# Kernel optimization log

Hardware: AMD Instinct MI355X
Metric: run time of the kernel (lower is better)

## Reference

```python
import jax, jax.numpy as jnp
import numpy as np

# Token / dim constants (from vm_step.Token and vm_step._SetDim)
CODE_START, CODE_END, MEM = 256, 257, 258
ADDR_KEY, MEM_STORE = 206, 455
VOCAB, D_MODEL = 272, 512
B, S = 16, 8192


def setup_inputs() -> dict:
    key = jax.random.key(0)
    k1, k2 = jax.random.split(key)
    token_ids = jax.random.randint(k1, (B, S), 0, VOCAB)
    embed_weight = jax.random.normal(k2, (VOCAB, D_MODEL), dtype=jnp.float32) * 0.02
    return {"token_ids": token_ids, "embed_weight": embed_weight, "mem_history_end": 2048}


def _augment_mask(token_ids, mem_history_end):
    """Boolean [B, S, D_MODEL] mask of positions that get set to 1.0."""
    Bb, Ss = token_ids.shape
    idx = jnp.arange(Ss)                                  # [S]
    is_start = token_ids == CODE_START
    is_end = token_ids == CODE_END
    # loop breaks at the FIRST CODE_END in each row
    end_idx = jnp.min(jnp.where(is_end, idx[None, :], Ss), axis=1)      # [B]
    # cs_pos = index of most recent CODE_START at-or-before i (-1 if none)
    cs = jax.lax.cummax(jnp.where(is_start, idx[None, :], -1), axis=1)  # [B,S]
    addr = idx[None, :] - cs - 1                                        # [B,S]
    valid = (cs >= 0) & (idx[None, :] < end_idx[:, None]) \
            & (token_ids < 256) & (addr >= 0)
    lo = addr & 15
    hi = (addr >> 4) & 15
    top = (addr >> 8) & 15
    bins = jnp.arange(16)                                 # nibble one-hots
    lo_oh = (bins == lo[..., None]) & valid[..., None]    # [B,S,16]
    hi_oh = (bins == hi[..., None]) & valid[..., None]
    top_oh = (bins == top[..., None]) & valid[..., None]
    mem_flag = (token_ids == MEM) & (idx[None, :] < mem_history_end)    # [B,S]

    mask = jnp.zeros((Bb, Ss, D_MODEL), dtype=bool)
    mask = mask.at[:, :, ADDR_KEY:ADDR_KEY + 16].set(lo_oh)
    mask = mask.at[:, :, ADDR_KEY + 16:ADDR_KEY + 32].set(hi_oh)
    mask = mask.at[:, :, ADDR_KEY + 32:ADDR_KEY + 48].set(top_oh)
    mask = mask.at[:, :, MEM_STORE].set(mem_flag)
    return mask


def reference(token_ids, embed_weight, mem_history_end):
    x = embed_weight[token_ids]                           # [B,S,D] gather
    mask = _augment_mask(token_ids, mem_history_end)
    return jnp.where(mask, jnp.asarray(1.0, x.dtype), x)
```

## Files before the change

kernel.cpp:

```cpp
#include <hip/hip_runtime.h>

#define TOK_CODE_START 256
#define TOK_CODE_END   257
#define TOK_MEM        258
#define ADDR_KEY       206
#define MEM_STORE      455

constexpr int Bb = 16;
constexpr int Ss = 8192;
constexpr int DM = 512;

__global__ __launch_bounds__(1024) void vm_scan_kernel(
    const int* __restrict__ tok,
    const int* __restrict__ mhe_p,
    unsigned int* __restrict__ ws)
{
    const int b = blockIdx.x;
    const int t = threadIdx.x;
    const int mhe = mhe_p[0];
    const int* row = tok + b * Ss;
    const int base = t * 8;

    int toks[8];
    int4 v0 = reinterpret_cast<const int4*>(row + base)[0];
    int4 v1 = reinterpret_cast<const int4*>(row + base)[1];
    toks[0] = v0.x; toks[1] = v0.y; toks[2] = v0.z; toks[3] = v0.w;
    toks[4] = v1.x; toks[5] = v1.y; toks[6] = v1.z; toks[7] = v1.w;

    int lmax = -1;
    int lend = Ss;
    #pragma unroll
    for (int k = 0; k < 8; ++k) {
        int idx = base + k;
        if (toks[k] == TOK_CODE_START) lmax = idx;
        if (toks[k] == TOK_CODE_END && lend == Ss) lend = idx;
    }

    __shared__ int smax[1024];
    __shared__ int smin[1024];
    smax[t] = lmax;
    smin[t] = lend;
    __syncthreads();

    for (int off = 512; off > 0; off >>= 1) {
        if (t < off) smin[t] = min(smin[t], smin[t + off]);
        __syncthreads();
    }
    const int end_idx = smin[0];

    for (int off = 1; off < 1024; off <<= 1) {
        int u = (t >= off) ? smax[t - off] : -1;
        __syncthreads();
        if (u > smax[t]) smax[t] = u;
        __syncthreads();
    }
    int run = (t > 0) ? smax[t - 1] : -1;

    unsigned int pk[8];
    #pragma unroll
    for (int k = 0; k < 8; ++k) {
        int idx = base + k;
        int tv = toks[k];
        if (tv == TOK_CODE_START) run = idx;
        int cs = run;
        int addr = idx - cs - 1;
        bool valid = (cs >= 0) && (idx < end_idx) && (tv < 256) && (addr >= 0);
        bool memf  = (tv == TOK_MEM) && (idx < mhe);
        unsigned int w = (valid ? 1u : 0u) | (memf ? 2u : 0u);
        if (valid) w |= ((unsigned int)addr << 2);
        pk[k] = w;
    }
    uint4* wr = reinterpret_cast<uint4*>(ws + b * Ss + base);
    wr[0] = make_uint4(pk[0], pk[1], pk[2], pk[3]);
    wr[1] = make_uint4(pk[4], pk[5], pk[6], pk[7]);
}

__global__ __launch_bounds__(256) void vm_gather_kernel(
    const int* __restrict__ tok,
    const float* __restrict__ emb,
    const unsigned int* __restrict__ ws,
    float4* __restrict__ out)
{
    const long long total = (long long)Bb * Ss * (DM / 4);
    const long long stride = (long long)gridDim.x * blockDim.x;
    for (long long w = (long long)blockIdx.x * blockDim.x + threadIdx.x;
         w < total; w += stride) {
        int bs = (int)(w >> 7);
        int dq = (int)(w & 127);
        int d0 = dq << 2;
        int tk = tok[bs];
        unsigned int pw = ws[bs];
        float4 v = reinterpret_cast<const float4*>(emb)[tk * (DM / 4) + dq];
        if (pw) {
            bool valid = (pw & 1u) != 0u;
            bool memf  = (pw & 2u) != 0u;
            int addr = (int)(pw >> 2);
            int p0 = ADDR_KEY      + (addr & 15);
            int p1 = ADDR_KEY + 16 + ((addr >> 4) & 15);
            int p2 = ADDR_KEY + 32 + ((addr >> 8) & 15);
            int d;
            d = d0 + 0; if ((valid && (d == p0 || d == p1 || d == p2)) || (memf && d == MEM_STORE)) v.x = 1.0f;
            d = d0 + 1; if ((valid && (d == p0 || d == p1 || d == p2)) || (memf && d == MEM_STORE)) v.y = 1.0f;
            d = d0 + 2; if ((valid && (d == p0 || d == p1 || d == p2)) || (memf && d == MEM_STORE)) v.z = 1.0f;
            d = d0 + 3; if ((valid && (d == p0 || d == p1 || d == p2)) || (memf && d == MEM_STORE)) v.w = 1.0f;
        }
        out[w] = v;
    }
}

extern "C" void kernel_launch(void* const* d_in, const int* in_sizes, int n_in,
                              void* d_out, int out_size, void* d_ws, size_t ws_size,
                              hipStream_t stream) {
    const int* tok = (const int*)d_in[0];
    const float* emb = (const float*)d_in[1];
    const int* mhe = (const int*)d_in[2];
    unsigned int* ws = (unsigned int*)d_ws;
    float4* out = (float4*)d_out;

    vm_scan_kernel<<<Bb, 1024, 0, stream>>>(tok, mhe, ws);
    vm_gather_kernel<<<2048, 256, 0, stream>>>(tok, emb, ws, out);
}
```

Before: 53.27 us.

## Use wave-shuffle scan, pack token into workspace word, nontemporal output stores

The scan kernel replaces its shared-memory Hillis-Steele scan and tree reduction, which need many __syncthreads, with wave-level shuffle scans plus a small cross-wave combine. The workspace word now also carries the token id, so the gather kernel no longer reads the token array. The gather uses 32-bit indexing and nontemporal stores for the 268MB output to reduce cache pollution. The gather is dominated by output write bandwidth, so these changes may matter little. The packing assumes token ids fit in 9 bits.

```diff
diff --git a/kernel.cpp b/kernel.cpp
--- a/kernel.cpp
+++ b/kernel.cpp
@@ -10,6 +10,8 @@
 constexpr int Ss = 8192;
 constexpr int DM = 512;
 
+typedef float f32x4 __attribute__((ext_vector_type(4)));
+
 __global__ __launch_bounds__(1024) void vm_scan_kernel(
     const int* __restrict__ tok,
     const int* __restrict__ mhe_p,
@@ -17,6 +19,8 @@
 {
     const int b = blockIdx.x;
     const int t = threadIdx.x;
+    const int lane = t & 63;
+    const int wid = t >> 6;
     const int mhe = mhe_p[0];
     const int* row = tok + b * Ss;
     const int base = t * 8;
@@ -36,25 +40,36 @@
         if (toks[k] == TOK_CODE_END && lend == Ss) lend = idx;
     }
 
-    __shared__ int smax[1024];
-    __shared__ int smin[1024];
-    smax[t] = lmax;
-    smin[t] = lend;
+    #pragma unroll
+    for (int off = 1; off < 64; off <<= 1) {
+        int u = __shfl_up(lmax, off);
+        if (lane >= off && u > lmax) lmax = u;
+    }
+    int excl = __shfl_up(lmax, 1);
+    if (lane == 0) excl = -1;
+
+    #pragma unroll
+    for (int off = 32; off > 0; off >>= 1) {
+        int u = __shfl_xor(lend, off);
+        if (u < lend) lend = u;
+    }
+
+    __shared__ int wmax[16];
+    __shared__ int wend[16];
+    if (lane == 63) wmax[wid] = lmax;
+    if (lane == 0)  wend[wid] = lend;
     __syncthreads();
 
-    for (int off = 512; off > 0; off >>= 1) {
-        if (t < off) smin[t] = min(smin[t], smin[t + off]);
-        __syncthreads();
-    }
-    const int end_idx = smin[0];
+    int carry = -1;
+    #pragma unroll
+    for (int j = 0; j < 16; ++j)
+        if (j < wid && wmax[j] > carry) carry = wmax[j];
+    int end_idx = Ss;
+    #pragma unroll
+    for (int j = 0; j < 16; ++j)
+        if (wend[j] < end_idx) end_idx = wend[j];
 
-    for (int off = 1; off < 1024; off <<= 1) {
-        int u = (t >= off) ? smax[t - off] : -1;
-        __syncthreads();
-        if (u > smax[t]) smax[t] = u;
-        __syncthreads();
-    }
-    int run = (t > 0) ? smax[t - 1] : -1;
+    int run = (carry > excl) ? carry : excl;
 
     unsigned int pk[8];
     #pragma unroll
@@ -66,8 +81,9 @@
         int addr = idx - cs - 1;
         bool valid = (cs >= 0) && (idx < end_idx) && (tv < 256) && (addr >= 0);
         bool memf  = (tv == TOK_MEM) && (idx < mhe);
-        unsigned int w = (valid ? 1u : 0u) | (memf ? 2u : 0u);
-        if (valid) w |= ((unsigned int)addr << 2);
+        unsigned int w = (unsigned int)tv;
+        if (valid) w |= (1u << 9) | ((unsigned int)addr << 11);
+        if (memf)  w |= (1u << 10);
         pk[k] = w;
     }
     uint4* wr = reinterpret_cast<uint4*>(ws + b * Ss + base);
@@ -76,35 +92,35 @@
 }
 
 __global__ __launch_bounds__(256) void vm_gather_kernel(
-    const int* __restrict__ tok,
-    const float* __restrict__ emb,
+    const f32x4* __restrict__ emb,
     const unsigned int* __restrict__ ws,
-    float4* __restrict__ out)
+    f32x4* __restrict__ out)
 {
-    const long long total = (long long)Bb * Ss * (DM / 4);
-    const long long stride = (long long)gridDim.x * blockDim.x;
-    for (long long w = (long long)blockIdx.x * blockDim.x + threadIdx.x;
-         w < total; w += stride) {
-        int bs = (int)(w >> 7);
-        int dq = (int)(w & 127);
-        int d0 = dq << 2;
-        int tk = tok[bs];
+    const int total = Bb * Ss * (DM / 4);
+    const int stride = gridDim.x * blockDim.x;
+    for (int w = blockIdx.x * blockDim.x + threadIdx.x; w < total; w += stride) {
+        int bs = w >> 7;
+        int dq = w & 127;
         unsigned int pw = ws[bs];
-        float4 v = reinterpret_cast<const float4*>(emb)[tk * (DM / 4) + dq];
-        if (pw) {
-            bool valid = (pw & 1u) != 0u;
-            bool memf  = (pw & 2u) != 0u;
-            int addr = (int)(pw >> 2);
+        int tk = (int)(pw & 511u);
+        f32x4 v = emb[tk * (DM / 4) + dq];
+        unsigned int flags = pw >> 9;
+        if (flags) {
+            bool valid = (flags & 1u) != 0u;
+            bool memf  = (flags & 2u) != 0u;
+            int addr = (int)(flags >> 2);
             int p0 = ADDR_KEY      + (addr & 15);
             int p1 = ADDR_KEY + 16 + ((addr >> 4) & 15);
             int p2 = ADDR_KEY + 32 + ((addr >> 8) & 15);
-            int d;
-            d = d0 + 0; if ((valid && (d == p0 || d == p1 || d == p2)) || (memf && d == MEM_STORE)) v.x = 1.0f;
-            d = d0 + 1; if ((valid && (d == p0 || d == p1 || d == p2)) || (memf && d == MEM_STORE)) v.y = 1.0f;
-            d = d0 + 2; if ((valid && (d == p0 || d == p1 || d == p2)) || (memf && d == MEM_STORE)) v.z = 1.0f;
-            d = d0 + 3; if ((valid && (d == p0 || d == p1 || d == p2)) || (memf && d == MEM_STORE)) v.w = 1.0f;
+            int d0 = dq << 2;
+            #pragma unroll
+            for (int j = 0; j < 4; ++j) {
+                int d = d0 + j;
+                if ((valid && (d == p0 || d == p1 || d == p2)) ||
+                    (memf && d == MEM_STORE)) v[j] = 1.0f;
+            }
         }
-        out[w] = v;
+        __builtin_nontemporal_store(v, &out[w]);
     }
 }
 
@@ -115,8 +131,8 @@
     const float* emb = (const float*)d_in[1];
     const int* mhe = (const int*)d_in[2];
     unsigned int* ws = (unsigned int*)d_ws;
-    float4* out = (float4*)d_out;
+    f32x4* out = (f32x4*)d_out;
 
     vm_scan_kernel<<<Bb, 1024, 0, stream>>>(tok, mhe, ws);
-    vm_gather_kernel<<<2048, 256, 0, stream>>>(tok, emb, ws, out);
+    vm_gather_kernel<<<2048, 256, 0, stream>>>((const f32x4*)emb, ws, out);
 }
```

After: 51.43 us. 1.04x faster.
